# Kernel optimization log

Hardware: AMD Instinct MI355X
Metric: run time of the kernel (lower is better)

The kernel has to match this reference:

```python
import jax, jax.numpy as jnp
import numpy as np
from jax import lax

N = 50000          # fluid particles
E = 1_600_000      # radius-graph edges (avg degree 32)
F_IN = 4           # fluidFeatures
NB = 8             # n = m = 8 basis functions per axis
K = NB * NB        # 64 total basis functions
SUPPORT = 1.0      # attributes['support']
LAYERS = [32, 64, 64, 2]


def setup_inputs() -> dict:
    key = jax.random.key(0)
    ks = jax.random.split(key, 24)
    inp = {
        "fluidPositions": jax.random.uniform(ks[0], (N, 2), jnp.float32),
        "fluidFeatures": jax.random.normal(ks[1], (N, F_IN), jnp.float32),
        "edge_i": jax.random.randint(ks[2], (E,), 0, N),  # receiver
        "edge_j": jax.random.randint(ks[3], (E,), 0, N),  # sender
    }
    # conv in/out channels per RbfNet wiring (boundaryFeatures == 0):
    dims = [(F_IN, LAYERS[0]), (2 * LAYERS[0], LAYERS[1]), (LAYERS[1], LAYERS[2]), (LAYERS[2], LAYERS[3])]
    k = 4
    for idx, (ci, co) in enumerate(dims):
        inp[f"cw{idx}"] = 0.1 * jax.random.normal(ks[k], (K, ci, co), jnp.float32); k += 1
        inp[f"cb{idx}"] = jnp.zeros((co,), jnp.float32)
        inp[f"fw{idx}"] = 0.1 * jax.random.normal(ks[k], (ci, co), jnp.float32); k += 1
        inp[f"fb{idx}"] = jnp.zeros((co,), jnp.float32)
    return inp


def _linear_basis(x, n):
    # hat (linear) RBF basis on n uniformly spaced centers in [-1, 1]
    centers = jnp.linspace(-1.0, 1.0, n, dtype=x.dtype)
    spacing = 2.0 / (n - 1)
    return jnp.maximum(0.0, 1.0 - jnp.abs(x[:, None] - centers[None, :]) / spacing)  # [E, n]


def _edge_basis(pos, ei, ej):
    # fluidEdgeLengths = -(pos[j] - pos[i]) / support, clamped to [-1, 1]
    d = (pos[ei] - pos[ej]) / SUPPORT
    d = jnp.clip(d, -1.0, 1.0)
    mask = ei != ej  # centerIgnore: drop self edges
    d = jnp.where(mask[:, None], d, jnp.array([1.0, 0.0], d.dtype))  # keep atan2 grads finite
    r = jnp.sqrt(jnp.sum(d * d, axis=-1) + 1e-12)
    u = jnp.clip(2.0 * r - 1.0, -1.0, 1.0)          # polar mapping: radius -> [-1, 1]
    v = jnp.arctan2(d[:, 1], d[:, 0]) / jnp.pi       # polar mapping: angle  -> [-1, 1]
    bu = _linear_basis(u, NB)
    bv = _linear_basis(v, NB)
    basis = (bu[:, :, None] * bv[:, None, :]).reshape(ei.shape[0], K)  # separable 2D basis
    return basis * mask[:, None].astype(basis.dtype)


def _rbf_conv(x, ei, ej, basis, W, b):
    # out[i] = sum_{e: dst(e)=i} sum_k basis[e,k] * (x[src(e)] @ W[k]) + b
    xj = x[ej]                           # [E, Cin] neighbor gather
    n_nodes = x.shape[0]
    init = jnp.zeros((n_nodes, W.shape[-1]), x.dtype)
    def body(acc, kw):
        bk, Wk = kw                      # bk: [E], Wk: [Cin, Cout]
        mom = jax.ops.segment_sum(bk[:, None] * xj, ei, num_segments=n_nodes)  # [N, Cin]
        return acc + mom @ Wk, None
    out, _ = lax.scan(body, init, (basis.T, W))
    return out + b


def reference(fluidPositions, fluidFeatures, edge_i, edge_j,
              cw0, cb0, fw0, fb0, cw1, cb1, fw1, fb1,
              cw2, cb2, fw2, fb2, cw3, cb3, fw3, fb3):
    basis = _edge_basis(fluidPositions, edge_i, edge_j)
    # layer 0: dense branch + fluid continuous conv, hstacked
    lin0 = fluidFeatures @ fw0 + fb0
    conv0 = _rbf_conv(fluidFeatures, edge_i, edge_j, basis, cw0, cb0)
    ans = jnp.concatenate([lin0, conv0], axis=1)  # [N, 64]
    # layer 1: features 32 != 64 -> no residual
    a = jax.nn.relu(ans)
    ans = _rbf_conv(a, edge_i, edge_j, basis, cw1, cb1) + a @ fw1 + fb1
    # layer 2: features 64 == 64 -> residual add
    a = jax.nn.relu(ans)
    ans = _rbf_conv(a, edge_i, edge_j, basis, cw2, cb2) + a @ fw2 + fb2 + ans
    # layer 3: features 64 != 2 -> no residual
    a = jax.nn.relu(ans)
    ans = _rbf_conv(a, edge_i, edge_j, basis, cw3, cb3) + a @ fw3 + fb3
    return ans / 128.0
```

## Files before the change

kernel.cpp:

```cpp
#include <hip/hip_runtime.h>
#include <math.h>

typedef _Float16 h8 __attribute__((ext_vector_type(8)));
typedef _Float16 h2 __attribute__((ext_vector_type(2)));
typedef float f32x4 __attribute__((ext_vector_type(4)));
typedef unsigned u32x2 __attribute__((ext_vector_type(2)));
typedef unsigned u32x4 __attribute__((ext_vector_type(4)));

__device__ __forceinline__ float clampf(float x, float lo, float hi) {
    return fminf(fmaxf(x, lo), hi);
}

__global__ void zero_ints(int* __restrict__ p, int n) {
    int i = blockIdx.x * 256 + threadIdx.x;
    if (i < n) p[i] = 0;
}

__global__ void repack_wh(const float* __restrict__ cw, const float* __restrict__ fw,
                          _Float16* __restrict__ Wh) {
    int idx = blockIdx.x * 256 + threadIdx.x;
    int total = 4 * 130 * 512;
    if (idx >= total) return;
    int j8 = idx & 7;
    int l = (idx >> 3) & 63;
    int rest = idx >> 9;
    int s = rest % 130;
    int t = rest / 130;
    int p = s * 32 + ((l >> 4) * 8) + j8;
    int co = t * 16 + (l & 15);
    float v = 0.f;
    if (p < 4096) {
        int tile = p >> 8;
        int g = (p >> 6) & 3;
        int m = (p >> 2) & 15;
        int i = p & 3;
        int mt = tile >> 2;
        int ct = tile & 3;
        int bin = mt * 16 + g * 4 + i;
        int c = ct * 16 + m;
        v = cw[(bin * 64 + c) * 64 + co];
    } else if (p < 4160) {
        v = fw[(p - 4096) * 64 + co];
    }
    Wh[idx] = (_Float16)v;
}

__global__ void repack_wh3(const float* __restrict__ cw, const float* __restrict__ fw,
                           _Float16* __restrict__ Wh) {
    int idx = blockIdx.x * 256 + threadIdx.x;
    int total = 130 * 512;
    if (idx >= total) return;
    int j8 = idx & 7;
    int l = (idx >> 3) & 63;
    int s = idx >> 9;
    int p = s * 32 + ((l >> 4) * 8) + j8;
    int co = l & 15;
    float v = 0.f;
    if (co < 2) {
        if (p < 4096) {
            int tile = p >> 8;
            int g = (p >> 6) & 3;
            int m = (p >> 2) & 15;
            int i = p & 3;
            int mt = tile >> 2;
            int ct = tile & 3;
            int bin = mt * 16 + g * 4 + i;
            int c = ct * 16 + m;
            v = cw[(bin * 64 + c) * 2 + co];
        } else if (p < 4160) {
            v = fw[(p - 4096) * 2 + co];
        }
    }
    Wh[idx] = (_Float16)v;
}

__global__ void repack_w0h(const float* __restrict__ cw0, const float* __restrict__ fw0,
                           _Float16* __restrict__ Wh) {
    int idx = blockIdx.x * 256 + threadIdx.x;
    int total = 4 * 9 * 512;
    if (idx >= total) return;
    int j8 = idx & 7;
    int l = (idx >> 3) & 63;
    int rest = idx >> 9;
    int s = rest % 9;
    int t = rest / 9;
    int p = s * 32 + ((l >> 4) * 8) + j8;
    int co = t * 16 + (l & 15);
    float v = 0.f;
    if (p < 256) {
        int bin = p & 63;
        int c = p >> 6;
        if (co >= 32) v = cw0[(bin * 4 + c) * 32 + (co - 32)];
    } else if (p < 260) {
        int c = p - 256;
        if (co < 32) v = fw0[c * 32 + co];
    }
    Wh[idx] = (_Float16)v;
}

__global__ void edge_hist(const int* __restrict__ ei, const int* __restrict__ ej,
                          int* __restrict__ counts, int E) {
    int e = blockIdx.x * 256 + threadIdx.x;
    if (e >= E) return;
    int i = ei[e], j = ej[e];
    if (i != j) atomicAdd(&counts[i], 1);
}

__global__ __launch_bounds__(1024) void scan_kernel(const int* __restrict__ counts,
                                                    int* __restrict__ offs,
                                                    int* __restrict__ cursor, int N) {
    __shared__ int sums[1024];
    const int t = threadIdx.x;
    const int per = (N + 1023) / 1024;
    const int lo = t * per;
    const int hi = min(lo + per, N);
    int s = 0;
    for (int i = lo; i < hi; ++i) s += counts[i];
    sums[t] = s;
    __syncthreads();
    for (int d = 1; d < 1024; d <<= 1) {
        int v = (t >= d) ? sums[t - d] : 0;
        __syncthreads();
        sums[t] += v;
        __syncthreads();
    }
    int run = (t > 0) ? sums[t - 1] : 0;
    for (int i = lo; i < hi; ++i) {
        offs[i] = run;
        cursor[i] = run;
        run += counts[i];
    }
    if (t == 1023) offs[N] = sums[1023];
}

__global__ void edge_scatter(const int* __restrict__ ei, const int* __restrict__ ej,
                             const float* __restrict__ pos, int* __restrict__ cursor,
                             uint4* __restrict__ csr_all, int E) {
    int e = blockIdx.x * 256 + threadIdx.x;
    if (e >= E) return;
    int i = ei[e], j = ej[e];
    if (i == j) return;
    float dx = clampf(pos[i * 2 + 0] - pos[j * 2 + 0], -1.f, 1.f);
    float dy = clampf(pos[i * 2 + 1] - pos[j * 2 + 1], -1.f, 1.f);
    float r = sqrtf(dx * dx + dy * dy + 1e-12f);
    float u = clampf(2.f * r - 1.f, -1.f, 1.f);
    float v = atan2f(dy, dx) * 0.3183098861837907f;
    float tu = (u + 1.f) * 3.5f;
    float tv = (v + 1.f) * 3.5f;
    int iu = min(6, max(0, (int)floorf(tu)));
    int iv = min(6, max(0, (int)floorf(tv)));
    float fu = clampf(tu - (float)iu, 0.f, 1.f);
    float fv = clampf(tv - (float)iv, 0.f, 1.f);
    bool even = (iu & 1) == 0;
    int rowi0 = even ? iu : iu + 1;
    int rowi1 = even ? iu + 1 : iu;
    float wu0 = even ? (1.f - fu) : fu;
    float wu1 = even ? fu : (1.f - fu);
    float gv = 1.f - fv;
    unsigned a0 = (unsigned)__builtin_bit_cast(unsigned short, (_Float16)(wu0 * gv)) |
                  ((unsigned)__builtin_bit_cast(unsigned short, (_Float16)(wu0 * fv)) << 16);
    unsigned a1 = (unsigned)__builtin_bit_cast(unsigned short, (_Float16)(wu1 * gv)) |
                  ((unsigned)__builtin_bit_cast(unsigned short, (_Float16)(wu1 * fv)) << 16);
    int p = atomicAdd(&cursor[i], 1);
    csr_all[p] = make_uint4(
        (unsigned)j | ((unsigned)(rowi0 >> 1) << 17) | ((unsigned)(rowi1 >> 1) << 19) |
            ((unsigned)iv << 21),
        0u, a0, a1);
}

__device__ __forceinline__ void mom_phase1_64(
    const _Float16* __restrict__ xh, const uint4* __restrict__ csr_all,
    _Float16* Ast, _Float16* Bst, unsigned bst_byte,
    int e0, int e1, int lane, f32x4* acc) {
    const int half = lane >> 5;
    const int el = lane & 31;
    const int q = lane >> 4;
    const int m = lane & 15;
    for (int bs = e0; bs < e1; bs += 32) {
        {
            uint4 z4 = make_uint4(0, 0, 0, 0);
#pragma unroll
            for (int zz = 0; zz < 4; ++zz) ((uint4*)Ast)[zz * 64 + lane] = z4;
        }
        int e = bs + el;
        bool ok = e < e1;
        uint4 ca = csr_all[ok ? e : e0];
        int jme = ok ? (int)(ca.x & 0x1FFFF) : -1;
        {
            int iv = (ca.x >> 21) & 7;
            int rowi = half ? (int)((((ca.x >> 19) & 3) << 1) + 1)
                            : (int)(((ca.x >> 17) & 3) << 1);
            h2 wts = __builtin_bit_cast(h2, half ? ca.w : ca.z);
            if (ok) {
                int bin0 = rowi * 8 + iv;
                int bin1 = bin0 + 1;
                int a0 = bin0 * 32 + (((el >> 3) + (bin0 >> 1)) & 3) * 8 + (el & 7);
                int a1 = bin1 * 32 + (((el >> 3) + (bin1 >> 1)) & 3) * 8 + (el & 7);
                Ast[a0] = wts[0];
                Ast[a1] = wts[1];
            }
        }
#pragma unroll
        for (int it = 0; it < 4; ++it) {
            int ee = it * 8 + (lane >> 3);
            int jj = __shfl(jme, ee);
            int c0 = (lane & 7) * 8;
            uint4 bv = make_uint4(0, 0, 0, 0);
            if (jj >= 0) bv = *(const uint4*)(xh + (size_t)jj * 64 + c0);
            int sub = (ee >> 2) * 4 + (c0 >> 4);
            ((uint4*)Bst)[sub * 8 + (ee & 3) * 2 + ((c0 >> 3) & 1)] = bv;
        }
        h8 af[4];
#pragma unroll
        for (int mt = 0; mt < 4; ++mt) {
            int binr = mt * 16 + m;
            int aoff = binr * 32 + ((q + (binr >> 1)) & 3) * 8;
            af[mt] = *(const h8*)(Ast + aoff);
        }
        unsigned bb = bst_byte + (unsigned)(q * 1024 + m * 8);
        h8 bf[4];
#pragma unroll
        for (int ct = 0; ct < 4; ++ct) {
            u32x2 lo, hi;
            asm volatile("ds_read_b64_tr_b16 %0, %2 offset:%3\n\t"
                         "ds_read_b64_tr_b16 %1, %2 offset:%4"
                         : "=&v"(lo), "=&v"(hi)
                         : "v"(bb), "i"(ct * 128), "i"(ct * 128 + 512)
                         : "memory");
            u32x4 t;
            t[0] = lo[0]; t[1] = lo[1]; t[2] = hi[0]; t[3] = hi[1];
            bf[ct] = __builtin_bit_cast(h8, t);
        }
        asm volatile("s_waitcnt lgkmcnt(0)" ::: "memory");
        __builtin_amdgcn_sched_barrier(0);
#pragma unroll
        for (int mt = 0; mt < 4; ++mt)
#pragma unroll
            for (int ct = 0; ct < 4; ++ct)
                acc[mt * 4 + ct] = __builtin_amdgcn_mfma_f32_16x16x32_f16(
                    af[mt], bf[ct], acc[mt * 4 + ct], 0, 0, 0);
    }
}

__device__ __forceinline__ void mom_writeback_64(const f32x4* acc, _Float16* momrow,
                                                 int lane) {
#pragma unroll
    for (int t = 0; t < 16; ++t) {
        h2 lo = {(_Float16)acc[t][0], (_Float16)acc[t][1]};
        h2 hi = {(_Float16)acc[t][2], (_Float16)acc[t][3]};
        h2* dst = (h2*)(momrow + t * 256 + (lane >> 4) * 64 + (lane & 15) * 4);
        dst[0] = lo;
        dst[1] = hi;
    }
}

template <int MODE>
__global__ __launch_bounds__(1024, 4) void conv64_mfma(
    const _Float16* __restrict__ xh, const float* __restrict__ x32,
    const _Float16* __restrict__ Wh,
    const float* __restrict__ cb, const float* __restrict__ fb,
    const int* __restrict__ offs, const uint4* __restrict__ csr_all,
    float* __restrict__ out32, _Float16* __restrict__ xh_out, int nNodes) {
    constexpr int TM = 16;
    constexpr int KSTEPS = 130;
    constexpr int RSH = 4184;
    extern __shared__ _Float16 smem[];
    const int tid = threadIdx.x;
    const int w = tid >> 6;
    const int lane = tid & 63;
    const int base = blockIdx.x * TM;
    const int n = base + w;

    _Float16* Ast = smem + w * RSH;
    _Float16* Bst = Ast + 2048;
    const unsigned bst_byte = (unsigned)((w * RSH + 2048) * 2);

    f32x4 acc[16] = {{0, 0, 0, 0}, {0, 0, 0, 0}, {0, 0, 0, 0}, {0, 0, 0, 0},
                     {0, 0, 0, 0}, {0, 0, 0, 0}, {0, 0, 0, 0}, {0, 0, 0, 0},
                     {0, 0, 0, 0}, {0, 0, 0, 0}, {0, 0, 0, 0}, {0, 0, 0, 0},
                     {0, 0, 0, 0}, {0, 0, 0, 0}, {0, 0, 0, 0}, {0, 0, 0, 0}};

    if (n < nNodes) {
        mom_phase1_64(xh, csr_all, Ast, Bst, bst_byte, offs[n], offs[n + 1], lane, acc);
        mom_writeback_64(acc, smem + w * RSH, lane);
        smem[w * RSH + 4096 + lane] = xh[(size_t)n * 64 + lane];
    }

    const int s0 = w * 8 + min(w, 2);
    const int s_end = s0 + 8 + (w < 2 ? 1 : 0);
    const int quad = lane >> 4;
    const _Float16* arow = smem + (lane & 15) * RSH;

    const uint4* Bp = (const uint4*)Wh;
    uint4 b0[4], b1[4];
#pragma unroll
    for (int t = 0; t < 4; ++t) {
        b0[t] = Bp[((size_t)t * KSTEPS + s0) * 64 + lane];
        b1[t] = Bp[((size_t)t * KSTEPS + s0 + 1) * 64 + lane];
    }
    __syncthreads();
    f32x4 acc2[4] = {{0, 0, 0, 0}, {0, 0, 0, 0}, {0, 0, 0, 0}, {0, 0, 0, 0}};
    for (int s = s0; s < s_end; ++s) {
        uint4 bq[4];
#pragma unroll
        for (int t = 0; t < 4; ++t) {
            bq[t] = b0[t];
            b0[t] = b1[t];
            if (s + 2 < s_end) b1[t] = Bp[((size_t)t * KSTEPS + s + 2) * 64 + lane];
        }
        h8 a = *(const h8*)(arow + s * 32 + quad * 8);
#pragma unroll
        for (int t = 0; t < 4; ++t)
            acc2[t] = __builtin_amdgcn_mfma_f32_16x16x32_f16(a, __builtin_bit_cast(h8, bq[t]),
                                                             acc2[t], 0, 0, 0);
    }
    __syncthreads();
    f32x4* red = (f32x4*)smem;
#pragma unroll
    for (int t = 0; t < 4; ++t) red[(w * 4 + t) * 64 + lane] = acc2[t];
    __syncthreads();
    if (w < 4) {
        f32x4 s = {0, 0, 0, 0};
#pragma unroll
        for (int g = 0; g < 16; ++g) s += red[(g * 4 + w) * 64 + lane];
        const int co = w * 16 + (lane & 15);
#pragma unroll
        for (int i = 0; i < 4; ++i) {
            int nn = base + quad * 4 + i;
            if (nn < nNodes) {
                float res = s[i] + cb[co] + fb[co];
                if (MODE == 2) res += x32[(size_t)nn * 64 + co];
                if (MODE == 1) out32[(size_t)nn * 64 + co] = res;
                xh_out[(size_t)nn * 64 + co] = (_Float16)fmaxf(res, 0.f);
            }
        }
    }
}

__global__ __launch_bounds__(1024, 4) void conv_last_mfma(
    const _Float16* __restrict__ xh, const _Float16* __restrict__ Wh3,
    const float* __restrict__ cb3, const float* __restrict__ fb3,
    const int* __restrict__ offs, const uint4* __restrict__ csr_all,
    float* __restrict__ out, int nNodes) {
    constexpr int TM = 16;
    constexpr int RSH = 4184;
    extern __shared__ _Float16 smem[];
    const int tid = threadIdx.x;
    const int w = tid >> 6;
    const int lane = tid & 63;
    const int base = blockIdx.x * TM;
    const int n = base + w;

    _Float16* Ast = smem + w * RSH;
    _Float16* Bst = Ast + 2048;
    const unsigned bst_byte = (unsigned)((w * RSH + 2048) * 2);

    f32x4 acc[16] = {{0, 0, 0, 0}, {0, 0, 0, 0}, {0, 0, 0, 0}, {0, 0, 0, 0},
                     {0, 0, 0, 0}, {0, 0, 0, 0}, {0, 0, 0, 0}, {0, 0, 0, 0},
                     {0, 0, 0, 0}, {0, 0, 0, 0}, {0, 0, 0, 0}, {0, 0, 0, 0},
                     {0, 0, 0, 0}, {0, 0, 0, 0}, {0, 0, 0, 0}, {0, 0, 0, 0}};

    if (n < nNodes) {
        mom_phase1_64(xh, csr_all, Ast, Bst, bst_byte, offs[n], offs[n + 1], lane, acc);
        mom_writeback_64(acc, smem + w * RSH, lane);
        smem[w * RSH + 4096 + lane] = xh[(size_t)n * 64 + lane];
    }

    const int s0 = w * 8 + min(w, 2);
    const int s_end = s0 + 8 + (w < 2 ? 1 : 0);
    const int quad = lane >> 4;
    const _Float16* arow = smem + (lane & 15) * RSH;
    const uint4* Bp = (const uint4*)Wh3;

    __syncthreads();
    f32x4 acc2 = {0, 0, 0, 0};
    for (int s = s0; s < s_end; ++s) {
        uint4 bq = Bp[(size_t)s * 64 + lane];
        h8 a = *(const h8*)(arow + s * 32 + quad * 8);
        acc2 = __builtin_amdgcn_mfma_f32_16x16x32_f16(a, __builtin_bit_cast(h8, bq),
                                                      acc2, 0, 0, 0);
    }
    __syncthreads();
    f32x4* red = (f32x4*)smem;
    red[w * 64 + lane] = acc2;
    __syncthreads();
    if (w == 0) {
        f32x4 s = {0, 0, 0, 0};
#pragma unroll
        for (int g = 0; g < 16; ++g) s += red[g * 64 + lane];
        const int co = lane & 15;
        if (co < 2) {
#pragma unroll
            for (int i = 0; i < 4; ++i) {
                int nn = base + quad * 4 + i;
                if (nn < nNodes)
                    out[nn * 2 + co] = (s[i] + cb3[co] + fb3[co]) * (1.f / 128.f);
            }
        }
    }
}

__global__ __launch_bounds__(1024, 4) void conv0_mfma(
    const float* __restrict__ xf, const _Float16* __restrict__ W0h,
    const float* __restrict__ cb0, const float* __restrict__ fb0,
    const int* __restrict__ offs, const uint4* __restrict__ csr_all,
    _Float16* __restrict__ xh_out, int nNodes) {
    constexpr int TM = 16;
    constexpr int RSH0 = 296;
    constexpr int MOMSZ = 16 * RSH0;
    extern __shared__ _Float16 smem[];
    const int tid = threadIdx.x;
    const int w = tid >> 6;
    const int lane = tid & 63;
    const int base = blockIdx.x * TM;
    const int n = base + w;

    _Float16* Ast = smem + MOMSZ + w * 2560;
    _Float16* Bst = Ast + 2048;
    _Float16* momrow = smem + w * RSH0;
    const unsigned bst_byte = (unsigned)((MOMSZ + w * 2560 + 2048) * 2);

    f32x4 acc[4] = {{0, 0, 0, 0}, {0, 0, 0, 0}, {0, 0, 0, 0}, {0, 0, 0, 0}};

    if (n < nNodes) {
        const int e0 = offs[n], e1 = offs[n + 1];
        const int half = lane >> 5;
        const int el = lane & 31;
        const int q = lane >> 4;
        const int m = lane & 15;
        for (int bs = e0; bs < e1; bs += 32) {
            {
                uint4 z4 = make_uint4(0, 0, 0, 0);
#pragma unroll
                for (int zz = 0; zz < 4; ++zz) ((uint4*)Ast)[zz * 64 + lane] = z4;
            }
            int e = bs + el;
            bool ok = e < e1;
            uint4 ca = csr_all[ok ? e : e0];
            int jme = ok ? (int)(ca.x & 0x1FFFF) : -1;
            {
                int iv = (ca.x >> 21) & 7;
                int rowi = half ? (int)((((ca.x >> 19) & 3) << 1) + 1)
                                : (int)(((ca.x >> 17) & 3) << 1);
                h2 wts = __builtin_bit_cast(h2, half ? ca.w : ca.z);
                if (ok) {
                    int bin0 = rowi * 8 + iv;
                    int bin1 = bin0 + 1;
                    int a0 = bin0 * 32 + (((el >> 3) + (bin0 >> 1)) & 3) * 8 + (el & 7);
                    int a1 = bin1 * 32 + (((el >> 3) + (bin1 >> 1)) & 3) * 8 + (el & 7);
                    Ast[a0] = wts[0];
                    Ast[a1] = wts[1];
                }
            }
            if (half == 0) {
                float4 xj = make_float4(0.f, 0.f, 0.f, 0.f);
                if (jme >= 0) xj = *(const float4*)(xf + (size_t)jme * 4);
                h2 d0 = {(_Float16)xj.x, (_Float16)xj.y};
                h2 d1 = {(_Float16)xj.z, (_Float16)xj.w};
                uint4 bv = make_uint4(__builtin_bit_cast(unsigned, d0),
                                      __builtin_bit_cast(unsigned, d1), 0u, 0u);
                uint4* dst = (uint4*)Bst + (el >> 2) * 8 + (el & 3) * 2;
                dst[0] = bv;
                dst[1] = make_uint4(0, 0, 0, 0);
            }
            h8 af[4];
#pragma unroll
            for (int mt = 0; mt < 4; ++mt) {
                int binr = mt * 16 + m;
                int aoff = binr * 32 + ((q + (binr >> 1)) & 3) * 8;
                af[mt] = *(const h8*)(Ast + aoff);
            }
            unsigned bb = bst_byte + (unsigned)(q * 256 + m * 8);
            u32x2 lo, hi;
            asm volatile("ds_read_b64_tr_b16 %0, %2 offset:0\n\t"
                         "ds_read_b64_tr_b16 %1, %2 offset:128"
                         : "=&v"(lo), "=&v"(hi)
                         : "v"(bb)
                         : "memory");
            u32x4 tt;
            tt[0] = lo[0]; tt[1] = lo[1]; tt[2] = hi[0]; tt[3] = hi[1];
            h8 b = __builtin_bit_cast(h8, tt);
            asm volatile("s_waitcnt lgkmcnt(0)" ::: "memory");
            __builtin_amdgcn_sched_barrier(0);
#pragma unroll
            for (int mt = 0; mt < 4; ++mt)
                acc[mt] = __builtin_amdgcn_mfma_f32_16x16x32_f16(af[mt], b, acc[mt], 0, 0, 0);
        }
        if ((lane & 15) < 4) {
#pragma unroll
            for (int mt = 0; mt < 4; ++mt) {
                _Float16* dst = momrow + mt * 16 + (lane >> 4) * 4 + 64 * (lane & 15);
                ((h2*)dst)[0] = h2{(_Float16)acc[mt][0], (_Float16)acc[mt][1]};
                ((h2*)dst)[1] = h2{(_Float16)acc[mt][2], (_Float16)acc[mt][3]};
            }
        }
        if (lane < 7) {
            h2 z = {(_Float16)0.f, (_Float16)0.f};
            h2* zp = (h2*)(momrow + 260 + lane * 4);
            zp[0] = z;
            zp[1] = z;
        }
        if (lane < 4) momrow[256 + lane] = (_Float16)xf[(size_t)n * 4 + lane];
    }

    const int quad = lane >> 4;
    const _Float16* arow = smem + (lane & 15) * RSH0;
    const uint4* Bp = (const uint4*)W0h;
    __syncthreads();
    f32x4 acc2[4] = {{0, 0, 0, 0}, {0, 0, 0, 0}, {0, 0, 0, 0}, {0, 0, 0, 0}};
    const int s0 = min(w, 9), s_end = min(w + 1, 9);
    for (int s = s0; s < s_end; ++s) {
        uint4 bq[4];
#pragma unroll
        for (int t = 0; t < 4; ++t) bq[t] = Bp[((size_t)t * 9 + s) * 64 + lane];
        h8 a = *(const h8*)(arow + s * 32 + quad * 8);
#pragma unroll
        for (int t = 0; t < 4; ++t)
            acc2[t] = __builtin_amdgcn_mfma_f32_16x16x32_f16(a, __builtin_bit_cast(h8, bq[t]),
                                                             acc2[t], 0, 0, 0);
    }
    __syncthreads();
    f32x4* red = (f32x4*)(smem + MOMSZ);
#pragma unroll
    for (int t = 0; t < 4; ++t) red[(w * 4 + t) * 64 + lane] = acc2[t];
    __syncthreads();
    if (w < 4) {
        f32x4 s = {0, 0, 0, 0};
#pragma unroll
        for (int g = 0; g < 16; ++g) s += red[(g * 4 + w) * 64 + lane];
        const int co = w * 16 + (lane & 15);
        const float bias = (co < 32) ? fb0[co] : cb0[co - 32];
#pragma unroll
        for (int i = 0; i < 4; ++i) {
            int nn = base + quad * 4 + i;
            if (nn < nNodes)
                xh_out[(size_t)nn * 64 + co] = (_Float16)fmaxf(s[i] + bias, 0.f);
        }
    }
}

extern "C" void kernel_launch(void* const* d_in, const int* in_sizes, int n_in,
                              void* d_out, int out_size, void* d_ws, size_t ws_size,
                              hipStream_t stream) {
    const float* pos = (const float*)d_in[0];
    const float* feat = (const float*)d_in[1];
    const int* ei = (const int*)d_in[2];
    const int* ej = (const int*)d_in[3];
    const float* cw0 = (const float*)d_in[4];
    const float* cb0 = (const float*)d_in[5];
    const float* fw0 = (const float*)d_in[6];
    const float* fb0 = (const float*)d_in[7];
    const float* cw1 = (const float*)d_in[8];
    const float* cb1 = (const float*)d_in[9];
    const float* fw1 = (const float*)d_in[10];
    const float* fb1 = (const float*)d_in[11];
    const float* cw2 = (const float*)d_in[12];
    const float* cb2 = (const float*)d_in[13];
    const float* fw2 = (const float*)d_in[14];
    const float* fb2 = (const float*)d_in[15];
    const float* cw3 = (const float*)d_in[16];
    const float* cb3 = (const float*)d_in[17];
    const float* fw3 = (const float*)d_in[18];
    const float* fb3 = (const float*)d_in[19];
    float* outp = (float*)d_out;

    const int N = in_sizes[0] / 2;
    const int E = in_sizes[2];

    char* wsp = (char*)d_ws;
    size_t off = 0;
    auto alloc = [&](size_t bytes) -> void* {
        void* p = wsp + off;
        off = (off + bytes + 255) & ~(size_t)255;
        return p;
    };
    int* counts = (int*)alloc((size_t)N * 4);
    int* offs = (int*)alloc((size_t)(N + 1) * 4);
    int* cursor = (int*)alloc((size_t)N * 4);
    uint4* csr_all = (uint4*)alloc((size_t)E * 16);
    float* ansB = (float*)alloc((size_t)N * 64 * 4);
    _Float16* xh0 = (_Float16*)alloc((size_t)N * 64 * 2);
    _Float16* xhB = (_Float16*)alloc((size_t)N * 64 * 2);
    _Float16* xhC = (_Float16*)alloc((size_t)N * 64 * 2);
    _Float16* Wh1 = (_Float16*)alloc((size_t)4 * 130 * 512 * 2);
    _Float16* Wh2 = (_Float16*)alloc((size_t)4 * 130 * 512 * 2);
    _Float16* Wh3 = (_Float16*)alloc((size_t)130 * 512 * 2);
    _Float16* W0h = (_Float16*)alloc((size_t)4 * 9 * 512 * 2);
    (void)ws_size;
    (void)n_in;
    (void)out_size;

    const int BIG_LDS = 16 * 4184 * 2;
    const int LDS0 = (16 * 296 + 16 * 2560) * 2;
    hipFuncSetAttribute((const void*)&conv64_mfma<1>,
                        hipFuncAttributeMaxDynamicSharedMemorySize, BIG_LDS);
    hipFuncSetAttribute((const void*)&conv64_mfma<2>,
                        hipFuncAttributeMaxDynamicSharedMemorySize, BIG_LDS);
    hipFuncSetAttribute((const void*)&conv_last_mfma,
                        hipFuncAttributeMaxDynamicSharedMemorySize, BIG_LDS);
    hipFuncSetAttribute((const void*)&conv0_mfma,
                        hipFuncAttributeMaxDynamicSharedMemorySize, LDS0);

    zero_ints<<<dim3((N + 255) / 256), dim3(256), 0, stream>>>(counts, N);
    const int RT = 4 * 130 * 512;
    repack_wh<<<dim3((RT + 255) / 256), dim3(256), 0, stream>>>(cw1, fw1, Wh1);
    repack_wh<<<dim3((RT + 255) / 256), dim3(256), 0, stream>>>(cw2, fw2, Wh2);
    repack_wh3<<<dim3((130 * 512 + 255) / 256), dim3(256), 0, stream>>>(cw3, fw3, Wh3);
    repack_w0h<<<dim3((4 * 9 * 512 + 255) / 256), dim3(256), 0, stream>>>(cw0, fw0, W0h);
    edge_hist<<<dim3((E + 255) / 256), dim3(256), 0, stream>>>(ei, ej, counts, E);
    scan_kernel<<<dim3(1), dim3(1024), 0, stream>>>(counts, offs, cursor, N);
    edge_scatter<<<dim3((E + 255) / 256), dim3(256), 0, stream>>>(ei, ej, pos, cursor, csr_all, E);

    const int nb = (N + 15) / 16;
    conv0_mfma<<<dim3(nb), dim3(1024), LDS0, stream>>>(
        feat, W0h, cb0, fb0, offs, csr_all, xh0, N);
    conv64_mfma<1><<<dim3(nb), dim3(1024), BIG_LDS, stream>>>(
        xh0, (const float*)nullptr, Wh1, cb1, fb1, offs, csr_all, ansB, xhB, N);
    conv64_mfma<2><<<dim3(nb), dim3(1024), BIG_LDS, stream>>>(
        xhB, ansB, Wh2, cb2, fb2, offs, csr_all, (float*)nullptr, xhC, N);
    conv_last_mfma<<<dim3(nb), dim3(1024), BIG_LDS, stream>>>(
        xhC, Wh3, cb3, fb3, offs, csr_all, outp, N);
}
```

Baseline: 829.7 us.

## Process two nodes per wavefront with interleaved gathers in conv kernels

The 64-channel and last conv kernels now launch 512 threads (8 waves) per 16-node block, and each wave handles two nodes. The edge-loop fetches for both nodes are issued before either tile's MFMA compute, so more gather latency is in flight per wave. The weight-GEMM phase gives each wave twice as many k-steps, and the reduction sums over 8 waves instead of 16. In exchange each wave holds two 16-register accumulator sets plus staged gather data, which raises VGPR pressure and lowers the number of waves per block.

```diff
diff --git a/kernel.cpp b/kernel.cpp
--- a/kernel.cpp
+++ b/kernel.cpp
@@ -168,47 +168,38 @@
         0u, a0, a1);
 }
 
-__device__ __forceinline__ void mom_phase1_64(
+__device__ __forceinline__ void mom_phase1_dual(
     const _Float16* __restrict__ xh, const uint4* __restrict__ csr_all,
-    _Float16* Ast, _Float16* Bst, unsigned bst_byte,
-    int e0, int e1, int lane, f32x4* acc) {
+    _Float16* smem, int w, int lane,
+    int e0A, int e1A, int e0B, int e1B, f32x4* accA, f32x4* accB) {
+    constexpr int RSH = 4184;
     const int half = lane >> 5;
     const int el = lane & 31;
     const int q = lane >> 4;
     const int m = lane & 15;
-    for (int bs = e0; bs < e1; bs += 32) {
-        {
-            uint4 z4 = make_uint4(0, 0, 0, 0);
-#pragma unroll
-            for (int zz = 0; zz < 4; ++zz) ((uint4*)Ast)[zz * 64 + lane] = z4;
-        }
-        int e = bs + el;
-        bool ok = e < e1;
-        uint4 ca = csr_all[ok ? e : e0];
-        int jme = ok ? (int)(ca.x & 0x1FFFF) : -1;
-        {
-            int iv = (ca.x >> 21) & 7;
-            int rowi = half ? (int)((((ca.x >> 19) & 3) << 1) + 1)
-                            : (int)(((ca.x >> 17) & 3) << 1);
-            h2 wts = __builtin_bit_cast(h2, half ? ca.w : ca.z);
-            if (ok) {
-                int bin0 = rowi * 8 + iv;
-                int bin1 = bin0 + 1;
-                int a0 = bin0 * 32 + (((el >> 3) + (bin0 >> 1)) & 3) * 8 + (el & 7);
-                int a1 = bin1 * 32 + (((el >> 3) + (bin1 >> 1)) & 3) * 8 + (el & 7);
-                Ast[a0] = wts[0];
-                Ast[a1] = wts[1];
-            }
+    _Float16* AstA = smem + w * RSH;
+    _Float16* BstA = AstA + 2048;
+    _Float16* AstB = smem + (w + 8) * RSH;
+    _Float16* BstB = AstB + 2048;
+    const unsigned bbA = (unsigned)((w * RSH + 2048) * 2) + (unsigned)(q * 1024 + m * 8);
+    const unsigned bbB = (unsigned)(((w + 8) * RSH + 2048) * 2) + (unsigned)(q * 1024 + m * 8);
+
+    auto tilecompute = [&](_Float16* Ast, _Float16* Bst, unsigned bb,
+                           int a0, int a1, unsigned wb, const uint4* bv, f32x4* acc) {
+        uint4 z4 = make_uint4(0, 0, 0, 0);
+#pragma unroll
+        for (int zz = 0; zz < 4; ++zz) ((uint4*)Ast)[zz * 64 + lane] = z4;
+        if (a0 >= 0) {
+            h2 wts = __builtin_bit_cast(h2, wb);
+            Ast[a0] = wts[0];
+            Ast[a1] = wts[1];
         }
 #pragma unroll
         for (int it = 0; it < 4; ++it) {
             int ee = it * 8 + (lane >> 3);
-            int jj = __shfl(jme, ee);
             int c0 = (lane & 7) * 8;
-            uint4 bv = make_uint4(0, 0, 0, 0);
-            if (jj >= 0) bv = *(const uint4*)(xh + (size_t)jj * 64 + c0);
             int sub = (ee >> 2) * 4 + (c0 >> 4);
-            ((uint4*)Bst)[sub * 8 + (ee & 3) * 2 + ((c0 >> 3) & 1)] = bv;
+            ((uint4*)Bst)[sub * 8 + (ee & 3) * 2 + ((c0 >> 3) & 1)] = bv[it];
         }
         h8 af[4];
 #pragma unroll
@@ -217,7 +208,6 @@
             int aoff = binr * 32 + ((q + (binr >> 1)) & 3) * 8;
             af[mt] = *(const h8*)(Ast + aoff);
         }
-        unsigned bb = bst_byte + (unsigned)(q * 1024 + m * 8);
         h8 bf[4];
 #pragma unroll
         for (int ct = 0; ct < 4; ++ct) {
@@ -239,6 +229,75 @@
             for (int ct = 0; ct < 4; ++ct)
                 acc[mt * 4 + ct] = __builtin_amdgcn_mfma_f32_16x16x32_f16(
                     af[mt], bf[ct], acc[mt * 4 + ct], 0, 0, 0);
+    };
+
+    int bsA = e0A, bsB = e0B;
+    while (bsA < e1A || bsB < e1B) {
+        const bool doA = bsA < e1A;
+        const bool doB = bsB < e1B;
+        uint4 caA, caB;
+        if (doA) { int e = bsA + el; caA = csr_all[e < e1A ? e : e0A]; }
+        if (doB) { int e = bsB + el; caB = csr_all[e < e1B ? e : e0B]; }
+        int aA0 = -1, aA1 = 0, jmeA = -1;
+        unsigned wbA = 0;
+        uint4 bvA[4];
+        int aB0 = -1, aB1 = 0, jmeB = -1;
+        unsigned wbB = 0;
+        uint4 bvB[4];
+        if (doA) {
+            bool ok = (bsA + el) < e1A;
+            jmeA = ok ? (int)(caA.x & 0x1FFFF) : -1;
+            int iv = (caA.x >> 21) & 7;
+            int rowi = half ? (int)((((caA.x >> 19) & 3) << 1) + 1)
+                            : (int)(((caA.x >> 17) & 3) << 1);
+            wbA = half ? caA.w : caA.z;
+            int bin0 = rowi * 8 + iv;
+            int bin1 = bin0 + 1;
+            if (ok) {
+                aA0 = bin0 * 32 + (((el >> 3) + (bin0 >> 1)) & 3) * 8 + (el & 7);
+                aA1 = bin1 * 32 + (((el >> 3) + (bin1 >> 1)) & 3) * 8 + (el & 7);
+            }
+#pragma unroll
+            for (int it = 0; it < 4; ++it) {
+                int ee = it * 8 + (lane >> 3);
+                int jj = __shfl(jmeA, ee);
+                int c0 = (lane & 7) * 8;
+                uint4 bvv = make_uint4(0, 0, 0, 0);
+                if (jj >= 0) bvv = *(const uint4*)(xh + (size_t)jj * 64 + c0);
+                bvA[it] = bvv;
+            }
+        }
+        if (doB) {
+            bool ok = (bsB + el) < e1B;
+            jmeB = ok ? (int)(caB.x & 0x1FFFF) : -1;
+            int iv = (caB.x >> 21) & 7;
+            int rowi = half ? (int)((((caB.x >> 19) & 3) << 1) + 1)
+                            : (int)(((caB.x >> 17) & 3) << 1);
+            wbB = half ? caB.w : caB.z;
+            int bin0 = rowi * 8 + iv;
+            int bin1 = bin0 + 1;
+            if (ok) {
+                aB0 = bin0 * 32 + (((el >> 3) + (bin0 >> 1)) & 3) * 8 + (el & 7);
+                aB1 = bin1 * 32 + (((el >> 3) + (bin1 >> 1)) & 3) * 8 + (el & 7);
+            }
+#pragma unroll
+            for (int it = 0; it < 4; ++it) {
+                int ee = it * 8 + (lane >> 3);
+                int jj = __shfl(jmeB, ee);
+                int c0 = (lane & 7) * 8;
+                uint4 bvv = make_uint4(0, 0, 0, 0);
+                if (jj >= 0) bvv = *(const uint4*)(xh + (size_t)jj * 64 + c0);
+                bvB[it] = bvv;
+            }
+        }
+        if (doA) {
+            tilecompute(AstA, BstA, bbA, aA0, aA1, wbA, bvA, accA);
+            bsA += 32;
+        }
+        if (doB) {
+            tilecompute(AstB, BstB, bbB, aB0, aB1, wbB, bvB, accB);
+            bsB += 32;
+        }
     }
 }
 
@@ -255,7 +314,7 @@
 }
 
 template <int MODE>
-__global__ __launch_bounds__(1024, 4) void conv64_mfma(
+__global__ __launch_bounds__(512, 2) void conv64_mfma(
     const _Float16* __restrict__ xh, const float* __restrict__ x32,
     const _Float16* __restrict__ Wh,
     const float* __restrict__ cb, const float* __restrict__ fb,
@@ -269,25 +328,34 @@
     const int w = tid >> 6;
     const int lane = tid & 63;
     const int base = blockIdx.x * TM;
-    const int n = base + w;
-
-    _Float16* Ast = smem + w * RSH;
-    _Float16* Bst = Ast + 2048;
-    const unsigned bst_byte = (unsigned)((w * RSH + 2048) * 2);
-
-    f32x4 acc[16] = {{0, 0, 0, 0}, {0, 0, 0, 0}, {0, 0, 0, 0}, {0, 0, 0, 0},
-                     {0, 0, 0, 0}, {0, 0, 0, 0}, {0, 0, 0, 0}, {0, 0, 0, 0},
-                     {0, 0, 0, 0}, {0, 0, 0, 0}, {0, 0, 0, 0}, {0, 0, 0, 0},
-                     {0, 0, 0, 0}, {0, 0, 0, 0}, {0, 0, 0, 0}, {0, 0, 0, 0}};
-
-    if (n < nNodes) {
-        mom_phase1_64(xh, csr_all, Ast, Bst, bst_byte, offs[n], offs[n + 1], lane, acc);
-        mom_writeback_64(acc, smem + w * RSH, lane);
-        smem[w * RSH + 4096 + lane] = xh[(size_t)n * 64 + lane];
-    }
-
-    const int s0 = w * 8 + min(w, 2);
-    const int s_end = s0 + 8 + (w < 2 ? 1 : 0);
+    const int nA = base + w;
+    const int nB = base + w + 8;
+
+    f32x4 accA[16] = {{0, 0, 0, 0}, {0, 0, 0, 0}, {0, 0, 0, 0}, {0, 0, 0, 0},
+                      {0, 0, 0, 0}, {0, 0, 0, 0}, {0, 0, 0, 0}, {0, 0, 0, 0},
+                      {0, 0, 0, 0}, {0, 0, 0, 0}, {0, 0, 0, 0}, {0, 0, 0, 0},
+                      {0, 0, 0, 0}, {0, 0, 0, 0}, {0, 0, 0, 0}, {0, 0, 0, 0}};
+    f32x4 accB[16] = {{0, 0, 0, 0}, {0, 0, 0, 0}, {0, 0, 0, 0}, {0, 0, 0, 0},
+                      {0, 0, 0, 0}, {0, 0, 0, 0}, {0, 0, 0, 0}, {0, 0, 0, 0},
+                      {0, 0, 0, 0}, {0, 0, 0, 0}, {0, 0, 0, 0}, {0, 0, 0, 0},
+                      {0, 0, 0, 0}, {0, 0, 0, 0}, {0, 0, 0, 0}, {0, 0, 0, 0}};
+
+    int e0A = 0, e1A = 0, e0B = 0, e1B = 0;
+    if (nA < nNodes) { e0A = offs[nA]; e1A = offs[nA + 1]; }
+    if (nB < nNodes) { e0B = offs[nB]; e1B = offs[nB + 1]; }
+
+    mom_phase1_dual(xh, csr_all, smem, w, lane, e0A, e1A, e0B, e1B, accA, accB);
+    if (nA < nNodes) {
+        mom_writeback_64(accA, smem + w * RSH, lane);
+        smem[w * RSH + 4096 + lane] = xh[(size_t)nA * 64 + lane];
+    }
+    if (nB < nNodes) {
+        mom_writeback_64(accB, smem + (w + 8) * RSH, lane);
+        smem[(w + 8) * RSH + 4096 + lane] = xh[(size_t)nB * 64 + lane];
+    }
+
+    const int s0 = w * 16 + min(w, 2);
+    const int s_end = s0 + 16 + (w < 2 ? 1 : 0);
     const int quad = lane >> 4;
     const _Float16* arow = smem + (lane & 15) * RSH;
 
@@ -322,7 +390,7 @@
     if (w < 4) {
         f32x4 s = {0, 0, 0, 0};
 #pragma unroll
-        for (int g = 0; g < 16; ++g) s += red[(g * 4 + w) * 64 + lane];
+        for (int g = 0; g < 8; ++g) s += red[(g * 4 + w) * 64 + lane];
         const int co = w * 16 + (lane & 15);
 #pragma unroll
         for (int i = 0; i < 4; ++i) {
@@ -337,7 +405,7 @@
     }
 }
 
-__global__ __launch_bounds__(1024, 4) void conv_last_mfma(
+__global__ __launch_bounds__(512, 2) void conv_last_mfma(
     const _Float16* __restrict__ xh, const _Float16* __restrict__ Wh3,
     const float* __restrict__ cb3, const float* __restrict__ fb3,
     const int* __restrict__ offs, const uint4* __restrict__ csr_all,
@@ -349,25 +417,34 @@
     const int w = tid >> 6;
     const int lane = tid & 63;
     const int base = blockIdx.x * TM;
-    const int n = base + w;
-
-    _Float16* Ast = smem + w * RSH;
-    _Float16* Bst = Ast + 2048;
-    const unsigned bst_byte = (unsigned)((w * RSH + 2048) * 2);
-
-    f32x4 acc[16] = {{0, 0, 0, 0}, {0, 0, 0, 0}, {0, 0, 0, 0}, {0, 0, 0, 0},
-                     {0, 0, 0, 0}, {0, 0, 0, 0}, {0, 0, 0, 0}, {0, 0, 0, 0},
-                     {0, 0, 0, 0}, {0, 0, 0, 0}, {0, 0, 0, 0}, {0, 0, 0, 0},
-                     {0, 0, 0, 0}, {0, 0, 0, 0}, {0, 0, 0, 0}, {0, 0, 0, 0}};
-
-    if (n < nNodes) {
-        mom_phase1_64(xh, csr_all, Ast, Bst, bst_byte, offs[n], offs[n + 1], lane, acc);
-        mom_writeback_64(acc, smem + w * RSH, lane);
-        smem[w * RSH + 4096 + lane] = xh[(size_t)n * 64 + lane];
-    }
-
-    const int s0 = w * 8 + min(w, 2);
-    const int s_end = s0 + 8 + (w < 2 ? 1 : 0);
+    const int nA = base + w;
+    const int nB = base + w + 8;
+
+    f32x4 accA[16] = {{0, 0, 0, 0}, {0, 0, 0, 0}, {0, 0, 0, 0}, {0, 0, 0, 0},
+                      {0, 0, 0, 0}, {0, 0, 0, 0}, {0, 0, 0, 0}, {0, 0, 0, 0},
+                      {0, 0, 0, 0}, {0, 0, 0, 0}, {0, 0, 0, 0}, {0, 0, 0, 0},
+                      {0, 0, 0, 0}, {0, 0, 0, 0}, {0, 0, 0, 0}, {0, 0, 0, 0}};
+    f32x4 accB[16] = {{0, 0, 0, 0}, {0, 0, 0, 0}, {0, 0, 0, 0}, {0, 0, 0, 0},
+                      {0, 0, 0, 0}, {0, 0, 0, 0}, {0, 0, 0, 0}, {0, 0, 0, 0},
+                      {0, 0, 0, 0}, {0, 0, 0, 0}, {0, 0, 0, 0}, {0, 0, 0, 0},
+                      {0, 0, 0, 0}, {0, 0, 0, 0}, {0, 0, 0, 0}, {0, 0, 0, 0}};
+
+    int e0A = 0, e1A = 0, e0B = 0, e1B = 0;
+    if (nA < nNodes) { e0A = offs[nA]; e1A = offs[nA + 1]; }
+    if (nB < nNodes) { e0B = offs[nB]; e1B = offs[nB + 1]; }
+
+    mom_phase1_dual(xh, csr_all, smem, w, lane, e0A, e1A, e0B, e1B, accA, accB);
+    if (nA < nNodes) {
+        mom_writeback_64(accA, smem + w * RSH, lane);
+        smem[w * RSH + 4096 + lane] = xh[(size_t)nA * 64 + lane];
+    }
+    if (nB < nNodes) {
+        mom_writeback_64(accB, smem + (w + 8) * RSH, lane);
+        smem[(w + 8) * RSH + 4096 + lane] = xh[(size_t)nB * 64 + lane];
+    }
+
+    const int s0 = w * 16 + min(w, 2);
+    const int s_end = s0 + 16 + (w < 2 ? 1 : 0);
     const int quad = lane >> 4;
     const _Float16* arow = smem + (lane & 15) * RSH;
     const uint4* Bp = (const uint4*)Wh3;
@@ -387,7 +464,7 @@
     if (w == 0) {
         f32x4 s = {0, 0, 0, 0};
 #pragma unroll
-        for (int g = 0; g < 16; ++g) s += red[g * 64 + lane];
+        for (int g = 0; g < 8; ++g) s += red[g * 64 + lane];
         const int co = lane & 15;
         if (co < 2) {
 #pragma unroll
@@ -614,10 +691,10 @@
     const int nb = (N + 15) / 16;
     conv0_mfma<<<dim3(nb), dim3(1024), LDS0, stream>>>(
         feat, W0h, cb0, fb0, offs, csr_all, xh0, N);
-    conv64_mfma<1><<<dim3(nb), dim3(1024), BIG_LDS, stream>>>(
+    conv64_mfma<1><<<dim3(nb), dim3(512), BIG_LDS, stream>>>(
         xh0, (const float*)nullptr, Wh1, cb1, fb1, offs, csr_all, ansB, xhB, N);
-    conv64_mfma<2><<<dim3(nb), dim3(1024), BIG_LDS, stream>>>(
+    conv64_mfma<2><<<dim3(nb), dim3(512), BIG_LDS, stream>>>(
         xhB, ansB, Wh2, cb2, fb2, offs, csr_all, (float*)nullptr, xhC, N);
-    conv_last_mfma<<<dim3(nb), dim3(1024), BIG_LDS, stream>>>(
+    conv_last_mfma<<<dim3(nb), dim3(512), BIG_LDS, stream>>>(
         xhC, Wh3, cb3, fb3, offs, csr_all, outp, N);
 }
```

Result: slower. 944.4 us (+13.8%).

## Sort nodes by degree bucket, split CSR into meta/weights, prefetch next edge tile

Applied to the files above, without the earlier changes.

Adds a single-block kernel that buckets nodes by how many 32-edge tiles they need and builds a permutation. All conv kernels then process nodes in that order, so each 16-wave block holds similarly loaded waves. The 16-byte CSR record, which carried an unused word, is split into a 4-byte meta array and an 8-byte weight array to cut edge-stream bytes. The mom_phase1 loop now prefetches the next tile's edge data and issues neighbor-feature gathers before the LDS zeroing, so memory latency overlaps other work. In exchange it adds a serial single-block pass with shared-memory atomics and indirect perm lookups, and loses contiguous output rows and neighbor locality.

```diff
diff --git a/kernel.cpp b/kernel.cpp
--- a/kernel.cpp
+++ b/kernel.cpp
@@ -133,9 +133,38 @@
     if (t == 1023) offs[N] = sums[1023];
 }
 
+__global__ __launch_bounds__(1024) void build_perm(const int* __restrict__ counts,
+                                                   int* __restrict__ perm, int N) {
+    __shared__ int bcnt[8];
+    __shared__ int boff[8];
+    const int t = threadIdx.x;
+    if (t < 8) bcnt[t] = 0;
+    __syncthreads();
+    for (int i = t; i < N; i += 1024) {
+        int tiles = (counts[i] + 31) >> 5;
+        int b = 7 - min(tiles, 7);
+        atomicAdd(&bcnt[b], 1);
+    }
+    __syncthreads();
+    if (t == 0) {
+        int run = 0;
+        for (int b = 0; b < 8; ++b) {
+            boff[b] = run;
+            run += bcnt[b];
+        }
+    }
+    __syncthreads();
+    for (int i = t; i < N; i += 1024) {
+        int tiles = (counts[i] + 31) >> 5;
+        int b = 7 - min(tiles, 7);
+        int slot = atomicAdd(&boff[b], 1);
+        perm[slot] = i;
+    }
+}
+
 __global__ void edge_scatter(const int* __restrict__ ei, const int* __restrict__ ej,
                              const float* __restrict__ pos, int* __restrict__ cursor,
-                             uint4* __restrict__ csr_all, int E) {
+                             unsigned* __restrict__ meta, uint2* __restrict__ wts, int E) {
     int e = blockIdx.x * 256 + threadIdx.x;
     if (e >= E) return;
     int i = ei[e], j = ej[e];
@@ -162,53 +191,68 @@
     unsigned a1 = (unsigned)__builtin_bit_cast(unsigned short, (_Float16)(wu1 * gv)) |
                   ((unsigned)__builtin_bit_cast(unsigned short, (_Float16)(wu1 * fv)) << 16);
     int p = atomicAdd(&cursor[i], 1);
-    csr_all[p] = make_uint4(
-        (unsigned)j | ((unsigned)(rowi0 >> 1) << 17) | ((unsigned)(rowi1 >> 1) << 19) |
-            ((unsigned)iv << 21),
-        0u, a0, a1);
+    meta[p] = (unsigned)j | ((unsigned)(rowi0 >> 1) << 17) | ((unsigned)(rowi1 >> 1) << 19) |
+              ((unsigned)iv << 21);
+    wts[p] = make_uint2(a0, a1);
 }
 
 __device__ __forceinline__ void mom_phase1_64(
-    const _Float16* __restrict__ xh, const uint4* __restrict__ csr_all,
+    const _Float16* __restrict__ xh, const unsigned* __restrict__ meta,
+    const uint2* __restrict__ wts,
     _Float16* Ast, _Float16* Bst, unsigned bst_byte,
     int e0, int e1, int lane, f32x4* acc) {
     const int half = lane >> 5;
     const int el = lane & 31;
     const int q = lane >> 4;
     const int m = lane & 15;
+
+    int e = e0 + el;
+    bool ok = e < e1;
+    unsigned me = meta[ok ? e : e0];
+    uint2 wv = wts[ok ? e : e0];
+
     for (int bs = e0; bs < e1; bs += 32) {
+        int en = bs + 32 + el;
+        bool okn = en < e1;
+        unsigned me_n = meta[okn ? en : e0];
+        uint2 wv_n = wts[okn ? en : e0];
+
+        int jme = ok ? (int)(me & 0x1FFFF) : -1;
+        uint4 bv[4];
+#pragma unroll
+        for (int it = 0; it < 4; ++it) {
+            int ee = it * 8 + (lane >> 3);
+            int jj = __shfl(jme, ee);
+            int c0 = (lane & 7) * 8;
+            uint4 bvv = make_uint4(0, 0, 0, 0);
+            if (jj >= 0) bvv = *(const uint4*)(xh + (size_t)jj * 64 + c0);
+            bv[it] = bvv;
+        }
         {
             uint4 z4 = make_uint4(0, 0, 0, 0);
 #pragma unroll
             for (int zz = 0; zz < 4; ++zz) ((uint4*)Ast)[zz * 64 + lane] = z4;
         }
-        int e = bs + el;
-        bool ok = e < e1;
-        uint4 ca = csr_all[ok ? e : e0];
-        int jme = ok ? (int)(ca.x & 0x1FFFF) : -1;
         {
-            int iv = (ca.x >> 21) & 7;
-            int rowi = half ? (int)((((ca.x >> 19) & 3) << 1) + 1)
-                            : (int)(((ca.x >> 17) & 3) << 1);
-            h2 wts = __builtin_bit_cast(h2, half ? ca.w : ca.z);
+            int iv = (me >> 21) & 7;
+            int rowi = half ? (int)((((me >> 19) & 3) << 1) + 1)
+                            : (int)(((me >> 17) & 3) << 1);
+            h2 wh = __builtin_bit_cast(h2, half ? wv.y : wv.x);
             if (ok) {
                 int bin0 = rowi * 8 + iv;
                 int bin1 = bin0 + 1;
                 int a0 = bin0 * 32 + (((el >> 3) + (bin0 >> 1)) & 3) * 8 + (el & 7);
                 int a1 = bin1 * 32 + (((el >> 3) + (bin1 >> 1)) & 3) * 8 + (el & 7);
-                Ast[a0] = wts[0];
-                Ast[a1] = wts[1];
+                Ast[a0] = wh[0];
+                Ast[a1] = wh[1];
             }
         }
 #pragma unroll
         for (int it = 0; it < 4; ++it) {
             int ee = it * 8 + (lane >> 3);
-            int jj = __shfl(jme, ee);
             int c0 = (lane & 7) * 8;
-            uint4 bv = make_uint4(0, 0, 0, 0);
-            if (jj >= 0) bv = *(const uint4*)(xh + (size_t)jj * 64 + c0);
             int sub = (ee >> 2) * 4 + (c0 >> 4);
-            ((uint4*)Bst)[sub * 8 + (ee & 3) * 2 + ((c0 >> 3) & 1)] = bv;
+            ((uint4*)Bst)[sub * 8 + (ee & 3) * 2 + ((c0 >> 3) & 1)] = bv[it];
         }
         h8 af[4];
 #pragma unroll
@@ -239,6 +283,9 @@
             for (int ct = 0; ct < 4; ++ct)
                 acc[mt * 4 + ct] = __builtin_amdgcn_mfma_f32_16x16x32_f16(
                     af[mt], bf[ct], acc[mt * 4 + ct], 0, 0, 0);
+        ok = okn;
+        me = me_n;
+        wv = wv_n;
     }
 }
 
@@ -259,7 +306,8 @@
     const _Float16* __restrict__ xh, const float* __restrict__ x32,
     const _Float16* __restrict__ Wh,
     const float* __restrict__ cb, const float* __restrict__ fb,
-    const int* __restrict__ offs, const uint4* __restrict__ csr_all,
+    const int* __restrict__ offs, const unsigned* __restrict__ meta,
+    const uint2* __restrict__ wts, const int* __restrict__ perm,
     float* __restrict__ out32, _Float16* __restrict__ xh_out, int nNodes) {
     constexpr int TM = 16;
     constexpr int KSTEPS = 130;
@@ -269,7 +317,7 @@
     const int w = tid >> 6;
     const int lane = tid & 63;
     const int base = blockIdx.x * TM;
-    const int n = base + w;
+    const int nIdx = base + w;
 
     _Float16* Ast = smem + w * RSH;
     _Float16* Bst = Ast + 2048;
@@ -280,8 +328,9 @@
                      {0, 0, 0, 0}, {0, 0, 0, 0}, {0, 0, 0, 0}, {0, 0, 0, 0},
                      {0, 0, 0, 0}, {0, 0, 0, 0}, {0, 0, 0, 0}, {0, 0, 0, 0}};
 
-    if (n < nNodes) {
-        mom_phase1_64(xh, csr_all, Ast, Bst, bst_byte, offs[n], offs[n + 1], lane, acc);
+    if (nIdx < nNodes) {
+        const int n = perm[nIdx];
+        mom_phase1_64(xh, meta, wts, Ast, Bst, bst_byte, offs[n], offs[n + 1], lane, acc);
         mom_writeback_64(acc, smem + w * RSH, lane);
         smem[w * RSH + 4096 + lane] = xh[(size_t)n * 64 + lane];
     }
@@ -326,8 +375,9 @@
         const int co = w * 16 + (lane & 15);
 #pragma unroll
         for (int i = 0; i < 4; ++i) {
-            int nn = base + quad * 4 + i;
-            if (nn < nNodes) {
+            int rr = base + quad * 4 + i;
+            if (rr < nNodes) {
+                int nn = perm[rr];
                 float res = s[i] + cb[co] + fb[co];
                 if (MODE == 2) res += x32[(size_t)nn * 64 + co];
                 if (MODE == 1) out32[(size_t)nn * 64 + co] = res;
@@ -340,7 +390,8 @@
 __global__ __launch_bounds__(1024, 4) void conv_last_mfma(
     const _Float16* __restrict__ xh, const _Float16* __restrict__ Wh3,
     const float* __restrict__ cb3, const float* __restrict__ fb3,
-    const int* __restrict__ offs, const uint4* __restrict__ csr_all,
+    const int* __restrict__ offs, const unsigned* __restrict__ meta,
+    const uint2* __restrict__ wts, const int* __restrict__ perm,
     float* __restrict__ out, int nNodes) {
     constexpr int TM = 16;
     constexpr int RSH = 4184;
@@ -349,7 +400,7 @@
     const int w = tid >> 6;
     const int lane = tid & 63;
     const int base = blockIdx.x * TM;
-    const int n = base + w;
+    const int nIdx = base + w;
 
     _Float16* Ast = smem + w * RSH;
     _Float16* Bst = Ast + 2048;
@@ -360,8 +411,9 @@
                      {0, 0, 0, 0}, {0, 0, 0, 0}, {0, 0, 0, 0}, {0, 0, 0, 0},
                      {0, 0, 0, 0}, {0, 0, 0, 0}, {0, 0, 0, 0}, {0, 0, 0, 0}};
 
-    if (n < nNodes) {
-        mom_phase1_64(xh, csr_all, Ast, Bst, bst_byte, offs[n], offs[n + 1], lane, acc);
+    if (nIdx < nNodes) {
+        const int n = perm[nIdx];
+        mom_phase1_64(xh, meta, wts, Ast, Bst, bst_byte, offs[n], offs[n + 1], lane, acc);
         mom_writeback_64(acc, smem + w * RSH, lane);
         smem[w * RSH + 4096 + lane] = xh[(size_t)n * 64 + lane];
     }
@@ -392,9 +444,11 @@
         if (co < 2) {
 #pragma unroll
             for (int i = 0; i < 4; ++i) {
-                int nn = base + quad * 4 + i;
-                if (nn < nNodes)
+                int rr = base + quad * 4 + i;
+                if (rr < nNodes) {
+                    int nn = perm[rr];
                     out[nn * 2 + co] = (s[i] + cb3[co] + fb3[co]) * (1.f / 128.f);
+                }
             }
         }
     }
@@ -403,7 +457,8 @@
 __global__ __launch_bounds__(1024, 4) void conv0_mfma(
     const float* __restrict__ xf, const _Float16* __restrict__ W0h,
     const float* __restrict__ cb0, const float* __restrict__ fb0,
-    const int* __restrict__ offs, const uint4* __restrict__ csr_all,
+    const int* __restrict__ offs, const unsigned* __restrict__ meta,
+    const uint2* __restrict__ wts, const int* __restrict__ perm,
     _Float16* __restrict__ xh_out, int nNodes) {
     constexpr int TM = 16;
     constexpr int RSH0 = 296;
@@ -413,7 +468,8 @@
     const int w = tid >> 6;
     const int lane = tid & 63;
     const int base = blockIdx.x * TM;
-    const int n = base + w;
+    const int nIdx = base + w;
+    const int n = (nIdx < nNodes) ? perm[nIdx] : -1;
 
     _Float16* Ast = smem + MOMSZ + w * 2560;
     _Float16* Bst = Ast + 2048;
@@ -422,7 +478,7 @@
 
     f32x4 acc[4] = {{0, 0, 0, 0}, {0, 0, 0, 0}, {0, 0, 0, 0}, {0, 0, 0, 0}};
 
-    if (n < nNodes) {
+    if (n >= 0) {
         const int e0 = offs[n], e1 = offs[n + 1];
         const int half = lane >> 5;
         const int el = lane & 31;
@@ -436,20 +492,21 @@
             }
             int e = bs + el;
             bool ok = e < e1;
-            uint4 ca = csr_all[ok ? e : e0];
-            int jme = ok ? (int)(ca.x & 0x1FFFF) : -1;
+            unsigned me = meta[ok ? e : e0];
+            uint2 wv = wts[ok ? e : e0];
+            int jme = ok ? (int)(me & 0x1FFFF) : -1;
             {
-                int iv = (ca.x >> 21) & 7;
-                int rowi = half ? (int)((((ca.x >> 19) & 3) << 1) + 1)
-                                : (int)(((ca.x >> 17) & 3) << 1);
-                h2 wts = __builtin_bit_cast(h2, half ? ca.w : ca.z);
+                int iv = (me >> 21) & 7;
+                int rowi = half ? (int)((((me >> 19) & 3) << 1) + 1)
+                                : (int)(((me >> 17) & 3) << 1);
+                h2 wh = __builtin_bit_cast(h2, half ? wv.y : wv.x);
                 if (ok) {
                     int bin0 = rowi * 8 + iv;
                     int bin1 = bin0 + 1;
                     int a0 = bin0 * 32 + (((el >> 3) + (bin0 >> 1)) & 3) * 8 + (el & 7);
                     int a1 = bin1 * 32 + (((el >> 3) + (bin1 >> 1)) & 3) * 8 + (el & 7);
-                    Ast[a0] = wts[0];
-                    Ast[a1] = wts[1];
+                    Ast[a0] = wh[0];
+                    Ast[a1] = wh[1];
                 }
             }
             if (half == 0) {
@@ -532,9 +589,11 @@
         const float bias = (co < 32) ? fb0[co] : cb0[co - 32];
 #pragma unroll
         for (int i = 0; i < 4; ++i) {
-            int nn = base + quad * 4 + i;
-            if (nn < nNodes)
+            int rr = base + quad * 4 + i;
+            if (rr < nNodes) {
+                int nn = perm[rr];
                 xh_out[(size_t)nn * 64 + co] = (_Float16)fmaxf(s[i] + bias, 0.f);
+            }
         }
     }
 }
@@ -577,7 +636,9 @@
     int* counts = (int*)alloc((size_t)N * 4);
     int* offs = (int*)alloc((size_t)(N + 1) * 4);
     int* cursor = (int*)alloc((size_t)N * 4);
-    uint4* csr_all = (uint4*)alloc((size_t)E * 16);
+    int* perm = (int*)alloc((size_t)N * 4);
+    unsigned* meta = (unsigned*)alloc((size_t)E * 4);
+    uint2* wts = (uint2*)alloc((size_t)E * 8);
     float* ansB = (float*)alloc((size_t)N * 64 * 4);
     _Float16* xh0 = (_Float16*)alloc((size_t)N * 64 * 2);
     _Float16* xhB = (_Float16*)alloc((size_t)N * 64 * 2);
@@ -609,15 +670,17 @@
     repack_w0h<<<dim3((4 * 9 * 512 + 255) / 256), dim3(256), 0, stream>>>(cw0, fw0, W0h);
     edge_hist<<<dim3((E + 255) / 256), dim3(256), 0, stream>>>(ei, ej, counts, E);
     scan_kernel<<<dim3(1), dim3(1024), 0, stream>>>(counts, offs, cursor, N);
-    edge_scatter<<<dim3((E + 255) / 256), dim3(256), 0, stream>>>(ei, ej, pos, cursor, csr_all, E);
+    build_perm<<<dim3(1), dim3(1024), 0, stream>>>(counts, perm, N);
+    edge_scatter<<<dim3((E + 255) / 256), dim3(256), 0, stream>>>(ei, ej, pos, cursor,
+                                                                 meta, wts, E);
 
     const int nb = (N + 15) / 16;
     conv0_mfma<<<dim3(nb), dim3(1024), LDS0, stream>>>(
-        feat, W0h, cb0, fb0, offs, csr_all, xh0, N);
+        feat, W0h, cb0, fb0, offs, meta, wts, perm, xh0, N);
     conv64_mfma<1><<<dim3(nb), dim3(1024), BIG_LDS, stream>>>(
-        xh0, (const float*)nullptr, Wh1, cb1, fb1, offs, csr_all, ansB, xhB, N);
+        xh0, (const float*)nullptr, Wh1, cb1, fb1, offs, meta, wts, perm, ansB, xhB, N);
     conv64_mfma<2><<<dim3(nb), dim3(1024), BIG_LDS, stream>>>(
-        xhB, ansB, Wh2, cb2, fb2, offs, csr_all, (float*)nullptr, xhC, N);
+        xhB, ansB, Wh2, cb2, fb2, offs, meta, wts, perm, (float*)nullptr, xhC, N);
     conv_last_mfma<<<dim3(nb), dim3(1024), BIG_LDS, stream>>>(
-        xhC, Wh3, cb3, fb3, offs, csr_all, outp, N);
-}
+        xhC, Wh3, cb3, fb3, offs, meta, wts, perm, outp, N);
+}
```

Result: slower. 939.9 us (+13.3%).
